# Kernel optimization log

Hardware: AMD Instinct MI355X
Metric: run time of the kernel (lower is better)

## Reference

```python
import jax, jax.numpy as jnp
import numpy as np

ALPHA = 4.0  # spikingjelly surrogate.Sigmoid default
V_TH = 1.0

@jax.custom_vjp
def spike_fn(x):
    # Heaviside: spike when membrane potential crosses threshold (x = v - V_TH)
    return (x >= 0.0).astype(x.dtype)

def _spike_fwd(x):
    return spike_fn(x), x

def _spike_bwd(x, g):
    s = jax.nn.sigmoid(ALPHA * x)
    return (g * ALPHA * s * (1.0 - s),)

spike_fn.defvjp(_spike_fwd, _spike_bwd)

def setup_inputs() -> dict:
    key = jax.random.key(0)
    k1, k2 = jax.random.split(key)
    T, B, F, O = 64, 2048, 784, 10
    x_spike = jax.random.uniform(k1, (T, B, F), dtype=jnp.float32)
    W = jax.random.normal(k2, (O, F), dtype=jnp.float32) * (1.0 / np.sqrt(F))
    b = jnp.zeros((O,), dtype=jnp.float32)
    return {"x_spike": x_spike, "W": W, "b": b}

def reference(x_spike, W, b):
    T, B, _ = x_spike.shape
    O = W.shape[0]

    def step(v, xt):
        c = jnp.dot(xt, W.T) + b              # [B, O] synaptic current
        v = v + c                              # IF neuron charge
        s = spike_fn(v - V_TH)                 # fire
        v = v * (1.0 - s)                      # hard reset to v_reset=0 (non-detached)
        return v, s

    v0 = jnp.zeros((B, O), dtype=x_spike.dtype)
    _, spikes = jax.lax.scan(step, v0, x_spike)  # spikes: [T, B, O]
    return spikes.mean(axis=0)                   # firing-rate output
```

## Files before the change

### kernel.cpp

```cpp
#include <hip/hip_runtime.h>


#define T_STEPS 64
#define BATCH   2048
#define FEAT    784
#define OUT_N   10
#define M_ROWS  (T_STEPS * BATCH)

__global__ __launch_bounds__(256)
void snn_gemm(const float* __restrict__ x, const float* __restrict__ W,
              const float* __restrict__ bias, float* __restrict__ C) {
    __shared__ float Wl[OUT_N * FEAT];

    for (int i = threadIdx.x; i < OUT_N * FEAT; i += 256) Wl[i] = W[i];
    __syncthreads();

    const int tid  = threadIdx.x;
    const int wave = tid >> 6;
    const int lane = tid & 63;
    const int l16  = lane & 15;
    const int r    = lane >> 4;
    const long gw   = (long)blockIdx.x * 4 + wave;
    const long row0 = gw * 16 + (long)r * 4;

    float acc[4][OUT_N];
#pragma unroll
    for (int g = 0; g < 4; ++g)
#pragma unroll
        for (int o = 0; o < OUT_N; ++o) acc[g][o] = 0.0f;

    const float* xbase = x + (size_t)row0 * FEAT + 4 * l16;

#pragma unroll
    for (int c = 0; c < 12; ++c) {
        float4 xf[4];
#pragma unroll
        for (int g = 0; g < 4; ++g)
            xf[g] = *(const float4*)(xbase + (size_t)g * FEAT + c * 64);
#pragma unroll
        for (int o = 0; o < OUT_N; ++o) {
            const float4 wf = *(const float4*)(&Wl[o * FEAT + 4 * l16 + c * 64]);
#pragma unroll
            for (int g = 0; g < 4; ++g) {
                acc[g][o] = fmaf(xf[g].x, wf.x, acc[g][o]);
                acc[g][o] = fmaf(xf[g].y, wf.y, acc[g][o]);
                acc[g][o] = fmaf(xf[g].z, wf.z, acc[g][o]);
                acc[g][o] = fmaf(xf[g].w, wf.w, acc[g][o]);
            }
        }
    }

    if (l16 < 4) {
#pragma unroll
        for (int g = 0; g < 4; ++g) {
            const float4 xt = *(const float4*)(xbase + (size_t)g * FEAT + 768);
#pragma unroll
            for (int o = 0; o < OUT_N; ++o) {
                const float4 wf = *(const float4*)(&Wl[o * FEAT + 768 + 4 * l16]);
                acc[g][o] = fmaf(xt.x, wf.x, acc[g][o]);
                acc[g][o] = fmaf(xt.y, wf.y, acc[g][o]);
                acc[g][o] = fmaf(xt.z, wf.z, acc[g][o]);
                acc[g][o] = fmaf(xt.w, wf.w, acc[g][o]);
            }
        }
    }

#pragma unroll
    for (int g = 0; g < 4; ++g)
#pragma unroll
        for (int o = 0; o < OUT_N; ++o) {
            float v = acc[g][o];
            v += __shfl_xor(v, 1, 64);
            v += __shfl_xor(v, 2, 64);
            v += __shfl_xor(v, 4, 64);
            v += __shfl_xor(v, 8, 64);
            acc[g][o] = v;
        }

    if (l16 == 0) {
#pragma unroll
        for (int g = 0; g < 4; ++g) {
            float* Cr = C + (size_t)(row0 + g) * OUT_N;
#pragma unroll
            for (int o = 0; o < OUT_N; ++o) Cr[o] = acc[g][o] + bias[o];
        }
    }
}

__global__ __launch_bounds__(256)
void snn_scan(const float* __restrict__ C, float* __restrict__ out) {
    const int idx = blockIdx.x * 256 + threadIdx.x;
    if (idx >= BATCH * OUT_N) return;
    float v = 0.0f;
    float cnt = 0.0f;
#pragma unroll
    for (int t = 0; t < T_STEPS; ++t) {
        v += C[(size_t)t * BATCH * OUT_N + idx];
        if (v >= 1.0f) { cnt += 1.0f; v = 0.0f; }
    }
    out[idx] = cnt * (1.0f / 64.0f);
}

extern "C" void kernel_launch(void* const* d_in, const int* in_sizes, int n_in,
                              void* d_out, int out_size, void* d_ws, size_t ws_size,
                              hipStream_t stream) {
    const float* x    = (const float*)d_in[0];
    const float* W    = (const float*)d_in[1];
    const float* bias = (const float*)d_in[2];
    float* out = (float*)d_out;
    float* C   = (float*)d_ws;

    snn_gemm<<<dim3(M_ROWS / 64), dim3(256), 0, stream>>>(x, W, bias, C);
    snn_scan<<<dim3((BATCH * OUT_N + 255) / 256), dim3(256), 0, stream>>>(C, out);
}
```

Baseline: 90.70 us.

## Fuse GEMM and IF scan per batch row with async LDS double-buffered x loads

Replaces the two-kernel GEMM-then-scan pipeline with a single kernel where each block owns one batch index across all 64 timesteps, keeps the per-step currents in shared memory, and runs the IF neuron scan in-block. This removes the intermediate C buffer round trip and the second launch. x tiles are streamed into LDS with global_load_lds in a double-buffered, XOR-swizzled layout, with explicit waitcnt pipelining. The risks are strided timestep access (rows 2048*784 floats apart), the larger LDS footprint limiting occupancy, and a serial 10-thread scan tail per block.

```diff
diff --git a/kernel.cpp b/kernel.cpp
--- a/kernel.cpp
+++ b/kernel.cpp
@@ -5,23 +5,53 @@
 #define BATCH   2048
 #define FEAT    784
 #define OUT_N   10
-#define M_ROWS  (T_STEPS * BATCH)
 
-__global__ __launch_bounds__(256)
-void snn_gemm(const float* __restrict__ x, const float* __restrict__ W,
-              const float* __restrict__ bias, float* __restrict__ C) {
-    __shared__ float Wl[OUT_N * FEAT];
+typedef __attribute__((address_space(1))) const void GV;
+typedef __attribute__((address_space(3))) void LV;
 
-    for (int i = threadIdx.x; i < OUT_N * FEAT; i += 256) Wl[i] = W[i];
+__device__ __forceinline__ void gld16(const float* src, float* dst) {
+    __builtin_amdgcn_global_load_lds((GV*)src, (LV*)dst, 16, 0, 0);
+}
+
+__global__ __launch_bounds__(256, 2)
+void snn_fused(const float* __restrict__ x, const float* __restrict__ W,
+               const float* __restrict__ bias, float* __restrict__ out) {
+    __shared__ float  Wl[OUT_N * FEAT];
+    __shared__ float4 xbuf[4][2][16][16];
+    __shared__ float4 xtail[4][16][4];
+    __shared__ float  c_sh[T_STEPS][12];
+
+    const int tid = threadIdx.x;
+    const int w   = tid >> 6;
+    const int ln  = tid & 63;
+    const int l16 = ln & 15;
+    const int r   = ln >> 4;
+    const int b   = blockIdx.x;
+
+#pragma unroll
+    for (int k = 0; k < 7; ++k)
+        gld16(W + (size_t)(k * 256 + tid) * 4, &Wl[(size_t)(k * 256 + w * 64) * 4]);
+    if (tid < 168)
+        gld16(W + (size_t)(1792 + tid) * 4, &Wl[(size_t)(1792 + w * 64) * 4]);
     __syncthreads();
 
-    const int tid  = threadIdx.x;
-    const int wave = tid >> 6;
-    const int lane = tid & 63;
-    const int l16  = lane & 15;
-    const int r    = lane >> 4;
-    const long gw   = (long)blockIdx.x * 4 + wave;
-    const long row0 = gw * 16 + (long)r * 4;
+    const size_t rowstride = (size_t)BATCH * FEAT;
+    const float* xb = x + (size_t)b * FEAT;
+
+    gld16(xb + (size_t)(w * 16 + (ln >> 2)) * rowstride + 768 + (ln & 3) * 4,
+          (float*)&xtail[w][0][0]);
+
+#define STAGE(c, bufi) do {                                                   \
+        _Pragma("unroll")                                                     \
+        for (int j = 0; j < 4; ++j) {                                         \
+            const int tp  = 4 * j + (ln >> 4);                                \
+            const int fqs = (ln & 15) ^ (j << 2);                             \
+            gld16(xb + (size_t)(w * 16 + tp) * rowstride + (c) * 64 + fqs * 4,\
+                  (float*)&xbuf[w][bufi][4 * j][0]);                          \
+        }                                                                     \
+    } while (0)
+
+    STAGE(0, 0);
 
     float acc[4][OUT_N];
 #pragma unroll
@@ -29,17 +59,24 @@
 #pragma unroll
         for (int o = 0; o < OUT_N; ++o) acc[g][o] = 0.0f;
 
-    const float* xbase = x + (size_t)row0 * FEAT + 4 * l16;
+#pragma unroll 1
+    for (int c = 0; c < 12; ++c) {
+        __builtin_amdgcn_sched_barrier(0);
+        if (c < 11) {
+            STAGE(c + 1, (c + 1) & 1);
+            asm volatile("s_waitcnt vmcnt(4)" ::: "memory");
+        } else {
+            asm volatile("s_waitcnt vmcnt(0)" ::: "memory");
+        }
+        __builtin_amdgcn_sched_barrier(0);
 
-#pragma unroll
-    for (int c = 0; c < 12; ++c) {
         float4 xf[4];
 #pragma unroll
         for (int g = 0; g < 4; ++g)
-            xf[g] = *(const float4*)(xbase + (size_t)g * FEAT + c * 64);
+            xf[g] = xbuf[w][c & 1][r * 4 + g][l16 ^ (r << 2)];
 #pragma unroll
         for (int o = 0; o < OUT_N; ++o) {
-            const float4 wf = *(const float4*)(&Wl[o * FEAT + 4 * l16 + c * 64]);
+            const float4 wf = *(const float4*)&Wl[o * FEAT + c * 64 + l16 * 4];
 #pragma unroll
             for (int g = 0; g < 4; ++g) {
                 acc[g][o] = fmaf(xf[g].x, wf.x, acc[g][o]);
@@ -51,16 +88,18 @@
     }
 
     if (l16 < 4) {
+        float4 xf[4];
 #pragma unroll
-        for (int g = 0; g < 4; ++g) {
-            const float4 xt = *(const float4*)(xbase + (size_t)g * FEAT + 768);
+        for (int g = 0; g < 4; ++g) xf[g] = xtail[w][r * 4 + g][l16];
 #pragma unroll
-            for (int o = 0; o < OUT_N; ++o) {
-                const float4 wf = *(const float4*)(&Wl[o * FEAT + 768 + 4 * l16]);
-                acc[g][o] = fmaf(xt.x, wf.x, acc[g][o]);
-                acc[g][o] = fmaf(xt.y, wf.y, acc[g][o]);
-                acc[g][o] = fmaf(xt.z, wf.z, acc[g][o]);
-                acc[g][o] = fmaf(xt.w, wf.w, acc[g][o]);
+        for (int o = 0; o < OUT_N; ++o) {
+            const float4 wf = *(const float4*)&Wl[o * FEAT + 768 + l16 * 4];
+#pragma unroll
+            for (int g = 0; g < 4; ++g) {
+                acc[g][o] = fmaf(xf[g].x, wf.x, acc[g][o]);
+                acc[g][o] = fmaf(xf[g].y, wf.y, acc[g][o]);
+                acc[g][o] = fmaf(xf[g].z, wf.z, acc[g][o]);
+                acc[g][o] = fmaf(xf[g].w, wf.w, acc[g][o]);
             }
         }
     }
@@ -80,25 +119,27 @@
     if (l16 == 0) {
 #pragma unroll
         for (int g = 0; g < 4; ++g) {
-            float* Cr = C + (size_t)(row0 + g) * OUT_N;
-#pragma unroll
-            for (int o = 0; o < OUT_N; ++o) Cr[o] = acc[g][o] + bias[o];
+            const int t = w * 16 + r * 4 + g;
+            *(float4*)&c_sh[t][0] = make_float4(acc[g][0], acc[g][1], acc[g][2], acc[g][3]);
+            *(float4*)&c_sh[t][4] = make_float4(acc[g][4], acc[g][5], acc[g][6], acc[g][7]);
+            *(float2*)&c_sh[t][8] = make_float2(acc[g][8], acc[g][9]);
         }
     }
-}
+    __syncthreads();
 
-__global__ __launch_bounds__(256)
-void snn_scan(const float* __restrict__ C, float* __restrict__ out) {
-    const int idx = blockIdx.x * 256 + threadIdx.x;
-    if (idx >= BATCH * OUT_N) return;
-    float v = 0.0f;
-    float cnt = 0.0f;
+    if (tid < OUT_N) {
+        const float bo = bias[tid];
+        float v = 0.0f, cnt = 0.0f;
 #pragma unroll
-    for (int t = 0; t < T_STEPS; ++t) {
-        v += C[(size_t)t * BATCH * OUT_N + idx];
-        if (v >= 1.0f) { cnt += 1.0f; v = 0.0f; }
+        for (int t = 0; t < T_STEPS; ++t) {
+            const float vv = v + c_sh[t][tid] + bo;
+            const bool  s  = (vv >= 1.0f);
+            cnt += s ? 1.0f : 0.0f;
+            v = s ? 0.0f : vv;
+        }
+        out[b * OUT_N + tid] = cnt * (1.0f / 64.0f);
     }
-    out[idx] = cnt * (1.0f / 64.0f);
+#undef STAGE
 }
 
 extern "C" void kernel_launch(void* const* d_in, const int* in_sizes, int n_in,
@@ -108,8 +149,6 @@
     const float* W    = (const float*)d_in[1];
     const float* bias = (const float*)d_in[2];
     float* out = (float*)d_out;
-    float* C   = (float*)d_ws;
 
-    snn_gemm<<<dim3(M_ROWS / 64), dim3(256), 0, stream>>>(x, W, bias, C);
-    snn_scan<<<dim3((BATCH * OUT_N + 255) / 256), dim3(256), 0, stream>>>(C, out);
+    snn_fused<<<dim3(BATCH), dim3(256), 0, stream>>>(x, W, bias, out);
 }
```

Result: slower. 95.72 us (+5.5%).

## Persistent GEMM blocks with double-buffered async global-to-LDS x tiles

Applied to the files above, without the earlier changes.

Replaces the one-shot grid of 2048 blocks, each reloading W into LDS, with 512 persistent blocks that loop over 16-row tiles. Each x tile is streamed into a double-buffered LDS region with global_load_lds so the next tile's load overlaps compute on the current one. The K dimension is split across the 4 waves, and partial sums are combined through LDS. Reductions use DPP instead of shuffles. The cost is higher LDS use (about 130KB, limiting occupancy to one block per CU), manual vmcnt bookkeeping, and extra barriers per tile.

```diff
diff --git a/kernel.cpp b/kernel.cpp
--- a/kernel.cpp
+++ b/kernel.cpp
@@ -5,84 +5,142 @@
 #define BATCH   2048
 #define FEAT    784
 #define OUT_N   10
-#define M_ROWS  (T_STEPS * BATCH)
+#define ROWS_TOTAL (T_STEPS * BATCH)
+#define TILE_ROWS  16
+#define TILE_FLTS  (TILE_ROWS * FEAT)
+#define NTILES     (ROWS_TOTAL / TILE_ROWS)
+#define NBLOCKS    512
+#define TPB        (NTILES / NBLOCKS)
+#define W_FLOATS   (OUT_N * FEAT)
+#define PART_FLTS  (4 * TILE_ROWS * OUT_N)
+#define SMEM_BYTES ((W_FLOATS + 2 * TILE_FLTS + PART_FLTS) * 4)
+
+typedef __attribute__((address_space(1))) const void GV;
+typedef __attribute__((address_space(3))) void LV;
+
+__device__ __forceinline__ void gld16(const float* src, float* dst) {
+    __builtin_amdgcn_global_load_lds((GV*)src, (LV*)dst, 16, 0, 0);
+}
+
+template <int CTRL>
+__device__ __forceinline__ float dpp_mov(float v) {
+    return __int_as_float(
+        __builtin_amdgcn_update_dpp(0, __float_as_int(v), CTRL, 0xF, 0xF, true));
+}
+__device__ __forceinline__ float red16(float v) {
+    v += dpp_mov<0xB1>(v);
+    v += dpp_mov<0x4E>(v);
+    v += dpp_mov<0x141>(v);
+    v += dpp_mov<0x140>(v);
+    return v;
+}
 
 __global__ __launch_bounds__(256)
 void snn_gemm(const float* __restrict__ x, const float* __restrict__ W,
               const float* __restrict__ bias, float* __restrict__ C) {
-    __shared__ float Wl[OUT_N * FEAT];
+    extern __shared__ float smem[];
+    float* Wl   = smem;
+    float* xb0  = smem + W_FLOATS;
+    float* xb1  = xb0 + TILE_FLTS;
+    float* part = xb1 + TILE_FLTS;
 
-    for (int i = threadIdx.x; i < OUT_N * FEAT; i += 256) Wl[i] = W[i];
+    const int tid = threadIdx.x;
+    const int w   = tid >> 6;
+    const int ln  = tid & 63;
+    const int l16 = ln & 15;
+    const int r   = ln >> 4;
+
+    for (int i = tid; i < W_FLOATS; i += 256) Wl[i] = W[i];
     __syncthreads();
 
-    const int tid  = threadIdx.x;
-    const int wave = tid >> 6;
-    const int lane = tid & 63;
-    const int l16  = lane & 15;
-    const int r    = lane >> 4;
-    const long gw   = (long)blockIdx.x * 4 + wave;
-    const long row0 = gw * 16 + (long)r * 4;
+    const float* xblk = x + (size_t)blockIdx.x * TPB * TILE_FLTS;
 
-    float acc[4][OUT_N];
+    auto stage = [&](int t, float* buf) {
+        const float* src = xblk + (size_t)t * TILE_FLTS + ln * 4;
 #pragma unroll
-    for (int g = 0; g < 4; ++g)
+        for (int i = 0; i < 12; ++i) {
+            const int k = 4 * i + w;
+            gld16(src + k * 256, buf + k * 256);
+        }
+        if (w == 0) gld16(src + 48 * 256, buf + 48 * 256);
+    };
+
+    stage(0, xb0);
+
+#pragma unroll 1
+    for (int t = 0; t < TPB; ++t) {
+        float* buf = (t & 1) ? xb1 : xb0;
+        if (t + 1 < TPB) {
+            stage(t + 1, (t & 1) ? xb0 : xb1);
+            if (w == 0) asm volatile("s_waitcnt vmcnt(13)" ::: "memory");
+            else        asm volatile("s_waitcnt vmcnt(12)" ::: "memory");
+        } else {
+            asm volatile("s_waitcnt vmcnt(0)" ::: "memory");
+        }
+        __builtin_amdgcn_s_barrier();
+
+        float acc[4][OUT_N];
 #pragma unroll
-        for (int o = 0; o < OUT_N; ++o) acc[g][o] = 0.0f;
-
-    const float* xbase = x + (size_t)row0 * FEAT + 4 * l16;
+        for (int g = 0; g < 4; ++g)
+#pragma unroll
+            for (int o = 0; o < OUT_N; ++o) acc[g][o] = 0.0f;
 
 #pragma unroll
-    for (int c = 0; c < 12; ++c) {
-        float4 xf[4];
+        for (int cc = 0; cc < 3; ++cc) {
+            const int c = w + 4 * cc;
+            float4 xf[4];
+#pragma unroll
+            for (int g = 0; g < 4; ++g)
+                xf[g] = *(const float4*)&buf[(4 * r + g) * FEAT + c * 64 + l16 * 4];
+#pragma unroll
+            for (int o = 0; o < OUT_N; ++o) {
+                const float4 wf = *(const float4*)&Wl[o * FEAT + c * 64 + l16 * 4];
+#pragma unroll
+                for (int g = 0; g < 4; ++g) {
+                    acc[g][o] = fmaf(xf[g].x, wf.x, acc[g][o]);
+                    acc[g][o] = fmaf(xf[g].y, wf.y, acc[g][o]);
+                    acc[g][o] = fmaf(xf[g].z, wf.z, acc[g][o]);
+                    acc[g][o] = fmaf(xf[g].w, wf.w, acc[g][o]);
+                }
+            }
+        }
+        if (w == 3 && l16 < 4) {
+#pragma unroll
+            for (int g = 0; g < 4; ++g) {
+                const float4 xt = *(const float4*)&buf[(4 * r + g) * FEAT + 768 + l16 * 4];
+#pragma unroll
+                for (int o = 0; o < OUT_N; ++o) {
+                    const float4 wf = *(const float4*)&Wl[o * FEAT + 768 + l16 * 4];
+                    acc[g][o] = fmaf(xt.x, wf.x, acc[g][o]);
+                    acc[g][o] = fmaf(xt.y, wf.y, acc[g][o]);
+                    acc[g][o] = fmaf(xt.z, wf.z, acc[g][o]);
+                    acc[g][o] = fmaf(xt.w, wf.w, acc[g][o]);
+                }
+            }
+        }
+
 #pragma unroll
         for (int g = 0; g < 4; ++g)
-            xf[g] = *(const float4*)(xbase + (size_t)g * FEAT + c * 64);
 #pragma unroll
-        for (int o = 0; o < OUT_N; ++o) {
-            const float4 wf = *(const float4*)(&Wl[o * FEAT + 4 * l16 + c * 64]);
+            for (int o = 0; o < OUT_N; ++o) acc[g][o] = red16(acc[g][o]);
+
+        if (l16 == 0) {
 #pragma unroll
             for (int g = 0; g < 4; ++g) {
-                acc[g][o] = fmaf(xf[g].x, wf.x, acc[g][o]);
-                acc[g][o] = fmaf(xf[g].y, wf.y, acc[g][o]);
-                acc[g][o] = fmaf(xf[g].z, wf.z, acc[g][o]);
-                acc[g][o] = fmaf(xf[g].w, wf.w, acc[g][o]);
+                float* p = &part[(w * TILE_ROWS + 4 * r + g) * OUT_N];
+                *(float4*)&p[0] = make_float4(acc[g][0], acc[g][1], acc[g][2], acc[g][3]);
+                *(float4*)&p[4] = make_float4(acc[g][4], acc[g][5], acc[g][6], acc[g][7]);
+                *(float2*)&p[8] = make_float2(acc[g][8], acc[g][9]);
             }
         }
-    }
+        asm volatile("s_waitcnt lgkmcnt(0)" ::: "memory");
+        __builtin_amdgcn_s_barrier();
 
-    if (l16 < 4) {
-#pragma unroll
-        for (int g = 0; g < 4; ++g) {
-            const float4 xt = *(const float4*)(xbase + (size_t)g * FEAT + 768);
-#pragma unroll
-            for (int o = 0; o < OUT_N; ++o) {
-                const float4 wf = *(const float4*)(&Wl[o * FEAT + 768 + 4 * l16]);
-                acc[g][o] = fmaf(xt.x, wf.x, acc[g][o]);
-                acc[g][o] = fmaf(xt.y, wf.y, acc[g][o]);
-                acc[g][o] = fmaf(xt.z, wf.z, acc[g][o]);
-                acc[g][o] = fmaf(xt.w, wf.w, acc[g][o]);
-            }
-        }
-    }
-
-#pragma unroll
-    for (int g = 0; g < 4; ++g)
-#pragma unroll
-        for (int o = 0; o < OUT_N; ++o) {
-            float v = acc[g][o];
-            v += __shfl_xor(v, 1, 64);
-            v += __shfl_xor(v, 2, 64);
-            v += __shfl_xor(v, 4, 64);
-            v += __shfl_xor(v, 8, 64);
-            acc[g][o] = v;
-        }
-
-    if (l16 == 0) {
-#pragma unroll
-        for (int g = 0; g < 4; ++g) {
-            float* Cr = C + (size_t)(row0 + g) * OUT_N;
-#pragma unroll
-            for (int o = 0; o < OUT_N; ++o) Cr[o] = acc[g][o] + bias[o];
+        if (tid < TILE_ROWS * OUT_N) {
+            const int o = tid % OUT_N;
+            const float s = part[tid] + part[160 + tid] + part[320 + tid] +
+                            part[480 + tid] + bias[o];
+            C[(size_t)(blockIdx.x * TPB + t) * (TILE_ROWS * OUT_N) + tid] = s;
         }
     }
 }
@@ -110,6 +168,9 @@
     float* out = (float*)d_out;
     float* C   = (float*)d_ws;
 
-    snn_gemm<<<dim3(M_ROWS / 64), dim3(256), 0, stream>>>(x, W, bias, C);
+    hipFuncSetAttribute(reinterpret_cast<const void*>(snn_gemm),
+                        hipFuncAttributeMaxDynamicSharedMemorySize, SMEM_BYTES);
+
+    snn_gemm<<<dim3(NBLOCKS), dim3(256), SMEM_BYTES, stream>>>(x, W, bias, C);
     snn_scan<<<dim3((BATCH * OUT_N + 255) / 256), dim3(256), 0, stream>>>(C, out);
 }
```

Result: slower. 130.7 us (+44.0%).
